# Kernel optimization log

Measured on AMD Instinct MI355X. Metric: run time of the kernel, lower is better.

## Reference

```python
import jax, jax.numpy as jnp
import numpy as np

B, L, H2 = 8, 512, 512  # batch, seq len (shared by a/b/c), 2*hidden


def setup_inputs() -> dict:
    key = jax.random.key(0)
    ka, kb, kc, kw1, kw2, kw3 = jax.random.split(key, 6)
    enc_a = jax.random.normal(ka, (B, L, H2), dtype=jnp.float32)
    enc_b = jax.random.normal(kb, (B, L, H2), dtype=jnp.float32)
    enc_c = jax.random.normal(kc, (B, L, H2), dtype=jnp.float32)
    # nn.Linear(6h, 1, bias=False) weight vectors; scaled so softmax isn't saturated
    w_ab = jax.random.normal(kw1, (3 * H2,), dtype=jnp.float32) * 0.02
    w_ac = jax.random.normal(kw2, (3 * H2,), dtype=jnp.float32) * 0.02
    w_bc = jax.random.normal(kw3, (3 * H2,), dtype=jnp.float32) * 0.02
    return {"encoded_a": enc_a, "encoded_b": enc_b, "encoded_c": enc_c,
            "w_ab": w_ab, "w_ac": w_ac, "w_bc": w_bc}


def _pair_att(A, Bx, w):
    """BiDAF-style pair attention.
    Original: S[b,i,j] = w . cat(A_i, B_j, A_i*B_j); here decomposed as
    S = A@w1 + B@w2 + A diag(w3) B^T  (identical math, no (B,La,Lb,6h) tensor).
    Returns a2b (B,La,2h) and b2a (B,2h) [pre-repeat].
    """
    h2 = A.shape[-1]
    wA, wB, wM = w[:h2], w[h2:2 * h2], w[2 * h2:]
    S = (A @ wA)[:, :, None] + (Bx @ wB)[:, None, :] \
        + jnp.einsum('bik,bjk->bij', A * wM, Bx)          # (B, La, Lb)
    a2b = jnp.einsum('bij,bjd->bid', jax.nn.softmax(S, axis=-1), Bx)  # (B, La, 2h)
    beta = jax.nn.softmax(jnp.max(S, axis=2), axis=-1)                # (B, La)
    b2a = jnp.einsum('bi,bid->bd', beta, A)                           # (B, 2h)
    return a2b, b2a


def reference(encoded_a, encoded_b, encoded_c, w_ab, w_ac, w_bc):
    b, len_b = encoded_b.shape[0], encoded_b.shape[1]
    len_c = encoded_c.shape[1]
    a2b, b2a = _pair_att(encoded_a, encoded_b, w_ab)
    a2c, c2a = _pair_att(encoded_a, encoded_c, w_ac)
    b2c, c2b = _pair_att(encoded_b, encoded_c, w_bc)
    # repeat the pooled vectors along the target sequence dim (as in torch .repeat)
    b2a = jnp.broadcast_to(b2a[:, None, :], (b, len_b, b2a.shape[-1]))
    c2a = jnp.broadcast_to(c2a[:, None, :], (b, len_c, c2a.shape[-1]))
    c2b = jnp.broadcast_to(c2b[:, None, :], (b, len_c, c2b.shape[-1]))
    att_a = jnp.concatenate((encoded_a, a2b, a2c, encoded_a * a2b, encoded_a * a2c), axis=2)
    att_b = jnp.concatenate((encoded_b, b2a, b2c, encoded_b * b2a, encoded_b * b2c), axis=2)
    att_c = jnp.concatenate((encoded_c, c2a, c2b, encoded_c * c2a, encoded_c * c2b), axis=2)
    return jnp.concatenate((att_a, att_b, att_c), axis=1)  # (B, La+Lb+Lc, 10h)
```

## Files before the change

kernel.cpp:

```cpp
#include <hip/hip_runtime.h>
#include <cmath>

#define BB 8
#define LL 512
#define HH 512

typedef __attribute__((ext_vector_type(8))) short short8;
typedef __attribute__((ext_vector_type(4))) float floatx4;

#define MM __builtin_amdgcn_mfma_f32_16x16x32_bf16
#define SB() __builtin_amdgcn_sched_barrier(0)

__device__ __forceinline__ unsigned short f2bf(float x) {
  unsigned int u = __float_as_uint(x);
  unsigned int r = (u + 0x7fffu + ((u >> 16) & 1u)) >> 16;
  return (unsigned short)r;
}

__global__ __launch_bounds__(256) void k0_conv(
    const float* __restrict__ Bm, const float* __restrict__ C,
    unsigned short* __restrict__ Bn, unsigned short* __restrict__ Cn,
    unsigned short* __restrict__ Bt, unsigned short* __restrict__ Ct) {
  __shared__ unsigned short tile[64][68];
  int bid = blockIdx.x;
  int s = bid >> 9;
  int rem = bid & 511;
  int b = rem >> 6, tr = (rem >> 3) & 7, tc = rem & 7;
  const float* src = s ? C : Bm;
  unsigned short* dn = s ? Cn : Bn;
  unsigned short* dt = s ? Ct : Bt;
  int t = threadIdx.x;
  int r0 = t >> 4, c0 = (t & 15) * 4;
#pragma unroll
  for (int rr = 0; rr < 4; ++rr) {
    int r = rr * 16 + r0;
    const float* sp = src + ((size_t)(b * 512 + tr * 64 + r)) * 512 + tc * 64 + c0;
    float4 v = *(const float4*)sp;
    unsigned short h0 = f2bf(v.x), h1 = f2bf(v.y), h2 = f2bf(v.z), h3 = f2bf(v.w);
    unsigned short* np = dn + ((size_t)(b * 512 + tr * 64 + r)) * 512 + tc * 64 + c0;
    np[0] = h0; np[1] = h1; np[2] = h2; np[3] = h3;
    tile[r][c0] = h0; tile[r][c0 + 1] = h1; tile[r][c0 + 2] = h2; tile[r][c0 + 3] = h3;
  }
  __syncthreads();
  int d = t & 63, j0 = (t >> 6) * 16;
  short8 v0, v1;
#pragma unroll
  for (int e = 0; e < 8; ++e) v0[e] = (short)tile[j0 + e][d];
#pragma unroll
  for (int e = 0; e < 8; ++e) v1[e] = (short)tile[j0 + 8 + e][d];
  unsigned short* tp = dt + ((size_t)(b * 512 + tc * 64 + d)) * 512 + tr * 64 + j0;
  *(short8*)tp = v0;
  *(short8*)(tp + 8) = v1;
}

__global__ __launch_bounds__(256) void k0_xm(
    const float* __restrict__ A, const float* __restrict__ Bm,
    const float* __restrict__ w0, const float* __restrict__ w1, const float* __restrict__ w2,
    unsigned short* __restrict__ Xm0, unsigned short* __restrict__ Xm1,
    unsigned short* __restrict__ Xm2) {
  unsigned int idx = blockIdx.x * 256 + threadIdx.x;
  size_t e0 = (size_t)idx * 8;
  int k0 = (int)(e0 & 511);
  unsigned int ri = (unsigned int)(e0 >> 9);
  int p = ri >> 12;
  unsigned int rowi = ri & 4095;
  const float* X = (p == 2) ? Bm : A;
  const float* wm = ((p == 0) ? w0 : (p == 1) ? w1 : w2) + 2 * HH;
  const float* xp = X + (size_t)rowi * 512 + k0;
  float4 a = *(const float4*)xp, b4 = *(const float4*)(xp + 4);
  float4 wa = *(const float4*)(wm + k0), wb = *(const float4*)(wm + k0 + 4);
  short8 o;
  o[0] = (short)f2bf(a.x * wa.x); o[1] = (short)f2bf(a.y * wa.y);
  o[2] = (short)f2bf(a.z * wa.z); o[3] = (short)f2bf(a.w * wa.w);
  o[4] = (short)f2bf(b4.x * wb.x); o[5] = (short)f2bf(b4.y * wb.y);
  o[6] = (short)f2bf(b4.z * wb.z); o[7] = (short)f2bf(b4.w * wb.w);
  unsigned short* op = ((p == 0) ? Xm0 : (p == 1) ? Xm1 : Xm2) + (size_t)rowi * 512 + k0;
  *(short8*)op = o;
}

__global__ __launch_bounds__(256) void k1_terms(
    const float* __restrict__ A, const float* __restrict__ Bm, const float* __restrict__ C,
    const float* __restrict__ w0, const float* __restrict__ w1, const float* __restrict__ w2,
    float* __restrict__ rowterm, float* __restrict__ colterm) {
  int tid = threadIdx.x;
  int wave = blockIdx.x * 4 + (tid >> 6);
  int lane = tid & 63;
  int m = wave >> 12;
  int rem = wave & 4095;
  int b = rem >> 9, i = rem & 511;
  const float* src = (m == 0) ? A : (m == 1 ? Bm : C);
  const float *wva, *wvb;
  float *da, *db;
  if (m == 0) {
    wva = w0;      wvb = w1;
    da = rowterm + (0 * BB + b) * LL + i;  db = rowterm + (1 * BB + b) * LL + i;
  } else if (m == 1) {
    wva = w0 + HH; wvb = w2;
    da = colterm + (0 * BB + b) * LL + i;  db = rowterm + (2 * BB + b) * LL + i;
  } else {
    wva = w1 + HH; wvb = w2 + HH;
    da = colterm + (1 * BB + b) * LL + i;  db = colterm + (2 * BB + b) * LL + i;
  }
  const float* row = src + ((size_t)b * LL + i) * HH;
  float a1 = 0.f, a2 = 0.f;
#pragma unroll
  for (int t = 0; t < 8; ++t) {
    float x = row[t * 64 + lane];
    a1 += x * wva[t * 64 + lane];
    a2 += x * wvb[t * 64 + lane];
  }
#pragma unroll
  for (int off = 32; off; off >>= 1) {
    a1 += __shfl_xor(a1, off, 64);
    a2 += __shfl_xor(a2, off, 64);
  }
  if (lane == 0) { *da = a1; *db = a2; }
}

__global__ __launch_bounds__(512, 2) void k2_mfma(
    const unsigned short* __restrict__ Xm0, const unsigned short* __restrict__ Xm1,
    const unsigned short* __restrict__ Xm2,
    const unsigned short* __restrict__ Bn, const unsigned short* __restrict__ Cn,
    const unsigned short* __restrict__ Bt, const unsigned short* __restrict__ Ct,
    const float* __restrict__ A, const float* __restrict__ Bm,
    const float* __restrict__ rowterm, const float* __restrict__ colterm,
    float* __restrict__ mrow, float* __restrict__ out) {
  __shared__ __align__(16) unsigned char smem[65536];
  unsigned short* A_lds = (unsigned short*)smem;
  unsigned short* P_lds = (unsigned short*)smem;
  float* sm_m = (float*)smem;
  float* sm_l = (float*)(smem + 2048);

  int tid = threadIdx.x;
  int bid0 = blockIdx.x;
  int bid = (bid0 & 7) * 24 + (bid0 >> 3);
  int p = bid >> 6;
  int b = (bid >> 3) & 7;
  int rb = bid & 7;
  int i0 = rb * 64;

  const unsigned short* Xmp = (p == 0) ? Xm0 : ((p == 1) ? Xm1 : Xm2);
  const unsigned short* Yn  = (p == 0) ? Bn : Cn;
  const unsigned short* Yt  = (p == 0) ? Bt : Ct;
  const float* X = (p == 2) ? Bm : A;

  int wc = tid >> 6;
  int lane = tid & 63;
  int n16 = lane & 15, q = lane >> 4;
  int e8 = n16 & 7;

#pragma unroll
  for (int j = 0; j < 8; ++j) {
    int idx = j * 512 + tid;
    int row = idx >> 6;
    int cc = idx & 63;
    short8 v = *(const short8*)(Xmp + ((size_t)(b * LL + i0 + row)) * HH + cc * 8);
    *(short8*)&A_lds[row * 512 + (cc ^ (row & 7)) * 8] = v;
  }
  __syncthreads();

  const unsigned short* br0 = Yn + ((size_t)(b * LL + wc * 64 + n16)) * HH + q * 8;
  const unsigned short* br1 = br0 + 16 * HH;
  const unsigned short* br2 = br0 + 32 * HH;
  const unsigned short* br3 = br0 + 48 * HH;

  floatx4 acc[4][4] = {};
  short8 Ax0[4], Ax1[4], Bx0[4], Bx1[4], Bx2[4];

#define LA(AF, kk) do { int ch_ = (((kk) * 4 + q) ^ e8) * 8; \
    AF[0] = *(const short8*)&A_lds[(n16)      * 512 + ch_]; \
    AF[1] = *(const short8*)&A_lds[(16 + n16) * 512 + ch_]; \
    AF[2] = *(const short8*)&A_lds[(32 + n16) * 512 + ch_]; \
    AF[3] = *(const short8*)&A_lds[(48 + n16) * 512 + ch_]; } while (0)
#define LB1(BF, kk) do { const int k0_ = (kk) * 32; \
    BF[0] = *(const short8*)(br0 + k0_); \
    BF[1] = *(const short8*)(br1 + k0_); \
    BF[2] = *(const short8*)(br2 + k0_); \
    BF[3] = *(const short8*)(br3 + k0_); } while (0)
#define MF1(AF, BF) do { \
    acc[0][0]=MM(AF[0],BF[0],acc[0][0],0,0,0); acc[0][1]=MM(AF[0],BF[1],acc[0][1],0,0,0); \
    acc[0][2]=MM(AF[0],BF[2],acc[0][2],0,0,0); acc[0][3]=MM(AF[0],BF[3],acc[0][3],0,0,0); \
    acc[1][0]=MM(AF[1],BF[0],acc[1][0],0,0,0); acc[1][1]=MM(AF[1],BF[1],acc[1][1],0,0,0); \
    acc[1][2]=MM(AF[1],BF[2],acc[1][2],0,0,0); acc[1][3]=MM(AF[1],BF[3],acc[1][3],0,0,0); \
    acc[2][0]=MM(AF[2],BF[0],acc[2][0],0,0,0); acc[2][1]=MM(AF[2],BF[1],acc[2][1],0,0,0); \
    acc[2][2]=MM(AF[2],BF[2],acc[2][2],0,0,0); acc[2][3]=MM(AF[2],BF[3],acc[2][3],0,0,0); \
    acc[3][0]=MM(AF[3],BF[0],acc[3][0],0,0,0); acc[3][1]=MM(AF[3],BF[1],acc[3][1],0,0,0); \
    acc[3][2]=MM(AF[3],BF[2],acc[3][2],0,0,0); acc[3][3]=MM(AF[3],BF[3],acc[3][3],0,0,0); } while (0)

  LB1(Bx0, 0); LB1(Bx1, 1); LB1(Bx2, 2); LA(Ax0, 0); LA(Ax1, 1); SB();
  MF1(Ax0, Bx0); LA(Ax0, 2);  LB1(Bx0, 3);  SB();
  MF1(Ax1, Bx1); LA(Ax1, 3);  LB1(Bx1, 4);  SB();
  MF1(Ax0, Bx2); LA(Ax0, 4);  LB1(Bx2, 5);  SB();
  MF1(Ax1, Bx0); LA(Ax1, 5);  LB1(Bx0, 6);  SB();
  MF1(Ax0, Bx1); LA(Ax0, 6);  LB1(Bx1, 7);  SB();
  MF1(Ax1, Bx2); LA(Ax1, 7);  LB1(Bx2, 8);  SB();
  MF1(Ax0, Bx0); LA(Ax0, 8);  LB1(Bx0, 9);  SB();
  MF1(Ax1, Bx1); LA(Ax1, 9);  LB1(Bx1, 10); SB();
  MF1(Ax0, Bx2); LA(Ax0, 10); LB1(Bx2, 11); SB();
  MF1(Ax1, Bx0); LA(Ax1, 11); LB1(Bx0, 12); SB();
  MF1(Ax0, Bx1); LA(Ax0, 12); LB1(Bx1, 13); SB();
  MF1(Ax1, Bx2); LA(Ax1, 13); LB1(Bx2, 14); SB();
  MF1(Ax0, Bx0); LA(Ax0, 14); LB1(Bx0, 15); SB();
  MF1(Ax1, Bx1); LA(Ax1, 15); SB();
  MF1(Ax0, Bx2); SB();
  MF1(Ax1, Bx0);
#undef LA
#undef LB1
#undef MF1

  __syncthreads();

  float rtv[4][4], ctv[4], mh[4][4], ml[4][4], rinv[4][4];
  {
    const float* rtp = rowterm + (p * BB + b) * LL + i0 + q * 4;
#pragma unroll
    for (int rt = 0; rt < 4; ++rt)
#pragma unroll
      for (int r = 0; r < 4; ++r) rtv[rt][r] = rtp[rt * 16 + r];
    const float* ctp = colterm + (p * BB + b) * LL + wc * 64 + n16;
#pragma unroll
    for (int f = 0; f < 4; ++f) ctv[f] = ctp[f * 16];
  }
#pragma unroll
  for (int rt = 0; rt < 4; ++rt)
#pragma unroll
    for (int r = 0; r < 4; ++r) {
      float m = -1e30f;
#pragma unroll
      for (int f = 0; f < 4; ++f) {
        float v = acc[rt][f][r] + rtv[rt][r] + ctv[f];
        acc[rt][f][r] = v;
        m = fmaxf(m, v);
      }
      m = fmaxf(m, __shfl_xor(m, 1, 64));
      m = fmaxf(m, __shfl_xor(m, 2, 64));
      m = fmaxf(m, __shfl_xor(m, 4, 64));
      m = fmaxf(m, __shfl_xor(m, 8, 64));
      mh[rt][r] = m;
    }
  if (n16 == 0) {
#pragma unroll
    for (int rt = 0; rt < 4; ++rt)
#pragma unroll
      for (int r = 0; r < 4; ++r) sm_m[wc * 64 + rt * 16 + q * 4 + r] = mh[rt][r];
  }
  __syncthreads();
#pragma unroll
  for (int rt = 0; rt < 4; ++rt)
#pragma unroll
    for (int r = 0; r < 4; ++r) {
      float m = mh[rt][r];
#pragma unroll
      for (int k = 0; k < 8; ++k) m = fmaxf(m, sm_m[k * 64 + rt * 16 + q * 4 + r]);
      mh[rt][r] = m;
      float l = 0.f;
#pragma unroll
      for (int f = 0; f < 4; ++f) {
        float pv = __expf(acc[rt][f][r] - m);
        acc[rt][f][r] = pv;
        l += pv;
      }
      l += __shfl_xor(l, 1, 64);
      l += __shfl_xor(l, 2, 64);
      l += __shfl_xor(l, 4, 64);
      l += __shfl_xor(l, 8, 64);
      ml[rt][r] = l;
    }
  if (n16 == 0) {
#pragma unroll
    for (int rt = 0; rt < 4; ++rt)
#pragma unroll
      for (int r = 0; r < 4; ++r) sm_l[wc * 64 + rt * 16 + q * 4 + r] = ml[rt][r];
    if (wc == 0) {
#pragma unroll
      for (int rt = 0; rt < 4; ++rt)
#pragma unroll
        for (int r = 0; r < 4; ++r)
          mrow[(p * BB + b) * LL + i0 + rt * 16 + q * 4 + r] = mh[rt][r];
    }
  }
  __syncthreads();
#pragma unroll
  for (int rt = 0; rt < 4; ++rt)
#pragma unroll
    for (int r = 0; r < 4; ++r) {
      float lf = 0.f;
#pragma unroll
      for (int k = 0; k < 8; ++k) lf += sm_l[k * 64 + rt * 16 + q * 4 + r];
      rinv[rt][r] = 1.f / lf;
    }
  __syncthreads();

#pragma unroll
  for (int f = 0; f < 4; ++f) {
    int c = wc * 8 + f * 2 + (n16 >> 3);
#pragma unroll
    for (int rt = 0; rt < 4; ++rt)
#pragma unroll
      for (int r = 0; r < 4; ++r) {
        int row = rt * 16 + q * 4 + r;
        int pc = c ^ (row & 7);
        P_lds[row * 512 + pc * 8 + e8] = f2bf(acc[rt][f][r]);
      }
  }
  __syncthreads();

  const unsigned short* tr0 = Yt + ((size_t)(b * LL + wc * 64 + n16)) * HH + q * 8;
  const unsigned short* tr1 = tr0 + 16 * HH;
  const unsigned short* tr2 = tr0 + 32 * HH;
  const unsigned short* tr3 = tr0 + 48 * HH;

  floatx4 oacc[4][4] = {};
  short8 Px0[4], Px1[4], By0[4], By1[4], By2[4];

#define LP(PF, kj) do { int ch_ = (((kj) * 4 + q) ^ e8) * 8; \
    PF[0] = *(const short8*)&P_lds[(n16)      * 512 + ch_]; \
    PF[1] = *(const short8*)&P_lds[(16 + n16) * 512 + ch_]; \
    PF[2] = *(const short8*)&P_lds[(32 + n16) * 512 + ch_]; \
    PF[3] = *(const short8*)&P_lds[(48 + n16) * 512 + ch_]; } while (0)
#define LB2(BF, kj) do { const int j0_ = (kj) * 32; \
    BF[0] = *(const short8*)(tr0 + j0_); \
    BF[1] = *(const short8*)(tr1 + j0_); \
    BF[2] = *(const short8*)(tr2 + j0_); \
    BF[3] = *(const short8*)(tr3 + j0_); } while (0)
#define MF2(PF, BF) do { \
    oacc[0][0]=MM(PF[0],BF[0],oacc[0][0],0,0,0); oacc[0][1]=MM(PF[0],BF[1],oacc[0][1],0,0,0); \
    oacc[0][2]=MM(PF[0],BF[2],oacc[0][2],0,0,0); oacc[0][3]=MM(PF[0],BF[3],oacc[0][3],0,0,0); \
    oacc[1][0]=MM(PF[1],BF[0],oacc[1][0],0,0,0); oacc[1][1]=MM(PF[1],BF[1],oacc[1][1],0,0,0); \
    oacc[1][2]=MM(PF[1],BF[2],oacc[1][2],0,0,0); oacc[1][3]=MM(PF[1],BF[3],oacc[1][3],0,0,0); \
    oacc[2][0]=MM(PF[2],BF[0],oacc[2][0],0,0,0); oacc[2][1]=MM(PF[2],BF[1],oacc[2][1],0,0,0); \
    oacc[2][2]=MM(PF[2],BF[2],oacc[2][2],0,0,0); oacc[2][3]=MM(PF[2],BF[3],oacc[2][3],0,0,0); \
    oacc[3][0]=MM(PF[3],BF[0],oacc[3][0],0,0,0); oacc[3][1]=MM(PF[3],BF[1],oacc[3][1],0,0,0); \
    oacc[3][2]=MM(PF[3],BF[2],oacc[3][2],0,0,0); oacc[3][3]=MM(PF[3],BF[3],oacc[3][3],0,0,0); } while (0)

  LB2(By0, 0); LB2(By1, 1); LB2(By2, 2); LP(Px0, 0); LP(Px1, 1); SB();
  MF2(Px0, By0); LP(Px0, 2);  LB2(By0, 3);  SB();
  MF2(Px1, By1); LP(Px1, 3);  LB2(By1, 4);  SB();
  MF2(Px0, By2); LP(Px0, 4);  LB2(By2, 5);  SB();
  MF2(Px1, By0); LP(Px1, 5);  LB2(By0, 6);  SB();
  MF2(Px0, By1); LP(Px0, 6);  LB2(By1, 7);  SB();
  MF2(Px1, By2); LP(Px1, 7);  LB2(By2, 8);  SB();
  MF2(Px0, By0); LP(Px0, 8);  LB2(By0, 9);  SB();
  MF2(Px1, By1); LP(Px1, 9);  LB2(By1, 10); SB();
  MF2(Px0, By2); LP(Px0, 10); LB2(By2, 11); SB();
  MF2(Px1, By0); LP(Px1, 11); LB2(By0, 12); SB();
  MF2(Px0, By1); LP(Px0, 12); LB2(By1, 13); SB();
  MF2(Px1, By2); LP(Px1, 13); LB2(By2, 14); SB();
  MF2(Px0, By0); LP(Px0, 14); LB2(By0, 15); SB();
  MF2(Px1, By1); LP(Px1, 15); SB();
  MF2(Px0, By2); SB();
  MF2(Px1, By0);
#undef LP
#undef LB2
#undef MF2

  int secoff, colbase;
  if      (p == 0) { secoff = 0;   colbase = 512;  }
  else if (p == 1) { secoff = 0;   colbase = 1024; }
  else             { secoff = 512; colbase = 1024; }

#pragma unroll
  for (int f = 0; f < 4; ++f) {
    int d = wc * 64 + f * 16 + n16;
#pragma unroll
    for (int rt = 0; rt < 4; ++rt)
#pragma unroll
      for (int r = 0; r < 4; ++r) {
        int ig = i0 + rt * 16 + q * 4 + r;
        float val = oacc[rt][f][r] * rinv[rt][r];
        size_t ob = ((size_t)b * 1536 + secoff + ig) * 2560;
        out[ob + colbase + d] = val;
        out[ob + colbase + 1024 + d] = X[((size_t)b * LL + ig) * HH + d] * val;
      }
  }
}

__global__ __launch_bounds__(256) void k3_beta(
    const float* __restrict__ A, const float* __restrict__ Bm,
    const float* __restrict__ mrow, float* __restrict__ vvec) {
  __shared__ float red[256];
  __shared__ float beta[LL];
  __shared__ float s_inv;
  int blk = blockIdx.x;
  int p = blk >> 6;
  int rem2 = blk & 63;
  int b = rem2 >> 3;
  int dch = rem2 & 7;
  int tid = threadIdx.x;
  const float* m = mrow + (p * BB + b) * LL;
  red[tid] = fmaxf(m[tid], m[tid + 256]);
  __syncthreads();
  for (int off = 128; off; off >>= 1) {
    if (tid < off) red[tid] = fmaxf(red[tid], red[tid + off]);
    __syncthreads();
  }
  float mx = red[0];
  __syncthreads();
  float e0 = __expf(m[tid] - mx), e1 = __expf(m[tid + 256] - mx);
  beta[tid] = e0; beta[tid + 256] = e1;
  red[tid] = e0 + e1;
  __syncthreads();
  for (int off = 128; off; off >>= 1) {
    if (tid < off) red[tid] += red[tid + off];
    __syncthreads();
  }
  if (tid == 0) s_inv = 1.f / red[0];
  __syncthreads();
  const float* Xb = ((p == 2) ? Bm : A) + (size_t)b * LL * HH;
  int d = dch * 64 + (tid & 63);
  int ig = tid >> 6;
  float acc = 0.f;
#pragma unroll 8
  for (int i = ig * 128; i < ig * 128 + 128; ++i)
    acc += beta[i] * Xb[(size_t)i * HH + d];
  red[tid] = acc;
  __syncthreads();
  if (tid < 64) {
    float s = red[tid] + red[tid + 64] + red[tid + 128] + red[tid + 192];
    vvec[(p * BB + b) * HH + dch * 64 + tid] = s * s_inv;
  }
}

__global__ __launch_bounds__(256) void k4_finalize(
    const float* __restrict__ A, const float* __restrict__ Bm, const float* __restrict__ C,
    const float* __restrict__ vvec, float* __restrict__ out) {
  unsigned int idx = blockIdx.x * 256 + threadIdx.x;
  int f4 = idx & 127;
  int i  = (idx >> 7) & 511;
  unsigned int ub = idx >> 16;
  unsigned int u = ub % 9;
  unsigned int b = ub / 9;
  int sec, slice;
  if (u == 0)      { sec = 0; slice = 0; }
  else if (u <= 3) { sec = 1; slice = (u == 1) ? 0 : (u == 2 ? 1 : 3); }
  else             { sec = 2; slice = (int)u - 4; }
  int cc = f4 * 4;
  const float* enc = sec == 0 ? A : (sec == 1 ? Bm : C);
  float4 val;
  if (slice == 0) {
    val = *(const float4*)(enc + ((size_t)b * LL + i) * HH + cc);
  } else {
    int vp = (sec == 1) ? 0 : ((slice == 1 || slice == 3) ? 1 : 2);
    float4 v = *(const float4*)(vvec + (vp * BB + b) * HH + cc);
    if (slice <= 2) {
      val = v;
    } else {
      float4 e = *(const float4*)(enc + ((size_t)b * LL + i) * HH + cc);
      val.x = e.x * v.x; val.y = e.y * v.y; val.z = e.z * v.z; val.w = e.w * v.w;
    }
  }
  *(float4*)(out + ((size_t)b * 1536 + sec * 512 + i) * 2560 + slice * 512 + cc) = val;
}

extern "C" void kernel_launch(void* const* d_in, const int* in_sizes, int n_in,
                              void* d_out, int out_size, void* d_ws, size_t ws_size,
                              hipStream_t stream) {
  const float* A  = (const float*)d_in[0];
  const float* Bm = (const float*)d_in[1];
  const float* C  = (const float*)d_in[2];
  const float* w0 = (const float*)d_in[3];
  const float* w1 = (const float*)d_in[4];
  const float* w2 = (const float*)d_in[5];
  float* out = (float*)d_out;

  float* wsf = (float*)d_ws;
  float* rowterm = wsf;
  float* colterm = wsf + 12288;
  float* mrow    = wsf + 24576;
  float* vvec    = wsf + 36864;
  unsigned short* wss = (unsigned short*)(wsf + 49152);
  const size_t MSZ = (size_t)BB * LL * HH;
  unsigned short* Bn  = wss;
  unsigned short* Cn  = wss + MSZ;
  unsigned short* Bt  = wss + 2 * MSZ;
  unsigned short* Ct  = wss + 3 * MSZ;
  unsigned short* Xm0 = wss + 4 * MSZ;
  unsigned short* Xm1 = wss + 5 * MSZ;
  unsigned short* Xm2 = wss + 6 * MSZ;

  k0_conv<<<1024, 256, 0, stream>>>(Bm, C, Bn, Cn, Bt, Ct);
  k0_xm<<<3072, 256, 0, stream>>>(A, Bm, w0, w1, w2, Xm0, Xm1, Xm2);
  k1_terms<<<3072, 256, 0, stream>>>(A, Bm, C, w0, w1, w2, rowterm, colterm);
  k2_mfma<<<192, 512, 0, stream>>>(Xm0, Xm1, Xm2, Bn, Cn, Bt, Ct, A, Bm,
                                   rowterm, colterm, mrow, out);
  k3_beta<<<192, 256, 0, stream>>>(A, Bm, mrow, vvec);
  k4_finalize<<<18432, 256, 0, stream>>>(A, Bm, C, vvec, out);
}
```

Measured before the change: 223.6 us.

## Fuse preprocessing passes and write encoder copies from the attention kernel

Merges the bf16 conversion, the Xm weight products and the row/column term dot products into a single pass that reads each fp32 row once with vectorized loads. The transpose kernel now reads bf16 instead of fp32. The attention kernel also writes the raw encoder slices for the a and b sections, which lets the finalize kernel drop two of its nine slice groups. k3_beta moves to 512 threads. The aim is to cut redundant fp32 reads of the inputs and extra output traffic, at the cost of more stores inside the MFMA kernel epilogue.

```diff
diff --git a/kernel.cpp b/kernel.cpp
--- a/kernel.cpp
+++ b/kernel.cpp
@@ -17,70 +17,12 @@
   return (unsigned short)r;
 }
 
-__global__ __launch_bounds__(256) void k0_conv(
-    const float* __restrict__ Bm, const float* __restrict__ C,
-    unsigned short* __restrict__ Bn, unsigned short* __restrict__ Cn,
-    unsigned short* __restrict__ Bt, unsigned short* __restrict__ Ct) {
-  __shared__ unsigned short tile[64][68];
-  int bid = blockIdx.x;
-  int s = bid >> 9;
-  int rem = bid & 511;
-  int b = rem >> 6, tr = (rem >> 3) & 7, tc = rem & 7;
-  const float* src = s ? C : Bm;
-  unsigned short* dn = s ? Cn : Bn;
-  unsigned short* dt = s ? Ct : Bt;
-  int t = threadIdx.x;
-  int r0 = t >> 4, c0 = (t & 15) * 4;
-#pragma unroll
-  for (int rr = 0; rr < 4; ++rr) {
-    int r = rr * 16 + r0;
-    const float* sp = src + ((size_t)(b * 512 + tr * 64 + r)) * 512 + tc * 64 + c0;
-    float4 v = *(const float4*)sp;
-    unsigned short h0 = f2bf(v.x), h1 = f2bf(v.y), h2 = f2bf(v.z), h3 = f2bf(v.w);
-    unsigned short* np = dn + ((size_t)(b * 512 + tr * 64 + r)) * 512 + tc * 64 + c0;
-    np[0] = h0; np[1] = h1; np[2] = h2; np[3] = h3;
-    tile[r][c0] = h0; tile[r][c0 + 1] = h1; tile[r][c0 + 2] = h2; tile[r][c0 + 3] = h3;
-  }
-  __syncthreads();
-  int d = t & 63, j0 = (t >> 6) * 16;
-  short8 v0, v1;
-#pragma unroll
-  for (int e = 0; e < 8; ++e) v0[e] = (short)tile[j0 + e][d];
-#pragma unroll
-  for (int e = 0; e < 8; ++e) v1[e] = (short)tile[j0 + 8 + e][d];
-  unsigned short* tp = dt + ((size_t)(b * 512 + tc * 64 + d)) * 512 + tr * 64 + j0;
-  *(short8*)tp = v0;
-  *(short8*)(tp + 8) = v1;
-}
-
-__global__ __launch_bounds__(256) void k0_xm(
-    const float* __restrict__ A, const float* __restrict__ Bm,
+__global__ __launch_bounds__(256) void kP1(
+    const float* __restrict__ A, const float* __restrict__ Bm, const float* __restrict__ C,
     const float* __restrict__ w0, const float* __restrict__ w1, const float* __restrict__ w2,
     unsigned short* __restrict__ Xm0, unsigned short* __restrict__ Xm1,
-    unsigned short* __restrict__ Xm2) {
-  unsigned int idx = blockIdx.x * 256 + threadIdx.x;
-  size_t e0 = (size_t)idx * 8;
-  int k0 = (int)(e0 & 511);
-  unsigned int ri = (unsigned int)(e0 >> 9);
-  int p = ri >> 12;
-  unsigned int rowi = ri & 4095;
-  const float* X = (p == 2) ? Bm : A;
-  const float* wm = ((p == 0) ? w0 : (p == 1) ? w1 : w2) + 2 * HH;
-  const float* xp = X + (size_t)rowi * 512 + k0;
-  float4 a = *(const float4*)xp, b4 = *(const float4*)(xp + 4);
-  float4 wa = *(const float4*)(wm + k0), wb = *(const float4*)(wm + k0 + 4);
-  short8 o;
-  o[0] = (short)f2bf(a.x * wa.x); o[1] = (short)f2bf(a.y * wa.y);
-  o[2] = (short)f2bf(a.z * wa.z); o[3] = (short)f2bf(a.w * wa.w);
-  o[4] = (short)f2bf(b4.x * wb.x); o[5] = (short)f2bf(b4.y * wb.y);
-  o[6] = (short)f2bf(b4.z * wb.z); o[7] = (short)f2bf(b4.w * wb.w);
-  unsigned short* op = ((p == 0) ? Xm0 : (p == 1) ? Xm1 : Xm2) + (size_t)rowi * 512 + k0;
-  *(short8*)op = o;
-}
-
-__global__ __launch_bounds__(256) void k1_terms(
-    const float* __restrict__ A, const float* __restrict__ Bm, const float* __restrict__ C,
-    const float* __restrict__ w0, const float* __restrict__ w1, const float* __restrict__ w2,
+    unsigned short* __restrict__ Xm2,
+    unsigned short* __restrict__ Bn, unsigned short* __restrict__ Cn,
     float* __restrict__ rowterm, float* __restrict__ colterm) {
   int tid = threadIdx.x;
   int wave = blockIdx.x * 4 + (tid >> 6);
@@ -89,6 +31,10 @@
   int rem = wave & 4095;
   int b = rem >> 9, i = rem & 511;
   const float* src = (m == 0) ? A : (m == 1 ? Bm : C);
+  const float* rp = src + (size_t)rem * HH + lane * 8;
+  float4 xa = *(const float4*)rp, xb = *(const float4*)(rp + 4);
+  float x[8] = {xa.x, xa.y, xa.z, xa.w, xb.x, xb.y, xb.z, xb.w};
+
   const float *wva, *wvb;
   float *da, *db;
   if (m == 0) {
@@ -101,20 +47,80 @@
     wva = w1 + HH; wvb = w2 + HH;
     da = colterm + (1 * BB + b) * LL + i;  db = colterm + (2 * BB + b) * LL + i;
   }
-  const float* row = src + ((size_t)b * LL + i) * HH;
+  const float* ap1 = wva + lane * 8;
+  const float* bp1 = wvb + lane * 8;
+  float4 wa1 = *(const float4*)ap1, wa2 = *(const float4*)(ap1 + 4);
+  float4 wb1 = *(const float4*)bp1, wb2 = *(const float4*)(bp1 + 4);
+  float wa[8] = {wa1.x, wa1.y, wa1.z, wa1.w, wa2.x, wa2.y, wa2.z, wa2.w};
+  float wb[8] = {wb1.x, wb1.y, wb1.z, wb1.w, wb2.x, wb2.y, wb2.z, wb2.w};
   float a1 = 0.f, a2 = 0.f;
 #pragma unroll
-  for (int t = 0; t < 8; ++t) {
-    float x = row[t * 64 + lane];
-    a1 += x * wva[t * 64 + lane];
-    a2 += x * wvb[t * 64 + lane];
-  }
+  for (int e = 0; e < 8; ++e) { a1 += x[e] * wa[e]; a2 += x[e] * wb[e]; }
 #pragma unroll
   for (int off = 32; off; off >>= 1) {
     a1 += __shfl_xor(a1, off, 64);
     a2 += __shfl_xor(a2, off, 64);
   }
   if (lane == 0) { *da = a1; *db = a2; }
+
+  size_t oo = (size_t)rem * HH + lane * 8;
+  if (m == 0) {
+    const float* m0 = w0 + 2 * HH + lane * 8;
+    const float* m1 = w1 + 2 * HH + lane * 8;
+    float4 ma1 = *(const float4*)m0, ma2 = *(const float4*)(m0 + 4);
+    float4 mb1 = *(const float4*)m1, mb2 = *(const float4*)(m1 + 4);
+    float wm0[8] = {ma1.x, ma1.y, ma1.z, ma1.w, ma2.x, ma2.y, ma2.z, ma2.w};
+    float wm1[8] = {mb1.x, mb1.y, mb1.z, mb1.w, mb2.x, mb2.y, mb2.z, mb2.w};
+    short8 o0, o1;
+#pragma unroll
+    for (int e = 0; e < 8; ++e) { o0[e] = (short)f2bf(x[e] * wm0[e]); o1[e] = (short)f2bf(x[e] * wm1[e]); }
+    *(short8*)(Xm0 + oo) = o0;
+    *(short8*)(Xm1 + oo) = o1;
+  } else if (m == 1) {
+    const float* m2 = w2 + 2 * HH + lane * 8;
+    float4 mc1 = *(const float4*)m2, mc2 = *(const float4*)(m2 + 4);
+    float wm2[8] = {mc1.x, mc1.y, mc1.z, mc1.w, mc2.x, mc2.y, mc2.z, mc2.w};
+    short8 on, o2;
+#pragma unroll
+    for (int e = 0; e < 8; ++e) { on[e] = (short)f2bf(x[e]); o2[e] = (short)f2bf(x[e] * wm2[e]); }
+    *(short8*)(Bn + oo) = on;
+    *(short8*)(Xm2 + oo) = o2;
+  } else {
+    short8 on;
+#pragma unroll
+    for (int e = 0; e < 8; ++e) on[e] = (short)f2bf(x[e]);
+    *(short8*)(Cn + oo) = on;
+  }
+}
+
+__global__ __launch_bounds__(256) void k0t(
+    const unsigned short* __restrict__ Bn, const unsigned short* __restrict__ Cn,
+    unsigned short* __restrict__ Bt, unsigned short* __restrict__ Ct) {
+  __shared__ unsigned short tile[64][68];
+  int bid = blockIdx.x;
+  int s = bid >> 9;
+  int rem = bid & 511;
+  int b = rem >> 6, tr = (rem >> 3) & 7, tc = rem & 7;
+  const unsigned short* src = s ? Cn : Bn;
+  unsigned short* dt = s ? Ct : Bt;
+  int t = threadIdx.x;
+#pragma unroll
+  for (int h = 0; h < 2; ++h) {
+    int id = h * 256 + t;
+    int row = id >> 3, c8 = id & 7;
+    short8 v = *(const short8*)(src + ((size_t)(b * 512 + tr * 64 + row)) * 512 + tc * 64 + c8 * 8);
+    *(short8*)&tile[row][c8 * 8] = v;
+  }
+  __syncthreads();
+  int d = t >> 2, jc = t & 3;
+  short8 v0, v1;
+#pragma unroll
+  for (int e = 0; e < 8; ++e) v0[e] = (short)tile[jc * 16 + e][d];
+#pragma unroll
+  for (int e = 0; e < 8; ++e) v1[e] = (short)tile[jc * 16 + 8 + e][d];
+  unsigned short* tp = dt + ((size_t)(b * 512 + tc * 64 + d)) * 512 + tr * 64 + jc * 16;
+  *(short8*)tp = v0;
+  *(short8*)(tp + 8) = v1;
 }
 
 __global__ __launch_bounds__(512, 2) void k2_mfma(
@@ -369,16 +375,19 @@
         int ig = i0 + rt * 16 + q * 4 + r;
         float val = oacc[rt][f][r] * rinv[rt][r];
         size_t ob = ((size_t)b * 1536 + secoff + ig) * 2560;
+        float xv = X[((size_t)b * LL + ig) * HH + d];
         out[ob + colbase + d] = val;
-        out[ob + colbase + 1024 + d] = X[((size_t)b * LL + ig) * HH + d] * val;
+        out[ob + colbase + 1024 + d] = xv * val;
+        if (p == 0) out[ob + d] = xv;
+        if (p == 2) out[ob + d] = xv;
       }
   }
 }
 
-__global__ __launch_bounds__(256) void k3_beta(
+__global__ __launch_bounds__(512) void k3_beta(
     const float* __restrict__ A, const float* __restrict__ Bm,
     const float* __restrict__ mrow, float* __restrict__ vvec) {
-  __shared__ float red[256];
+  __shared__ float red[512];
   __shared__ float beta[LL];
   __shared__ float s_inv;
   int blk = blockIdx.x;
@@ -388,19 +397,19 @@
   int dch = rem2 & 7;
   int tid = threadIdx.x;
   const float* m = mrow + (p * BB + b) * LL;
-  red[tid] = fmaxf(m[tid], m[tid + 256]);
-  __syncthreads();
-  for (int off = 128; off; off >>= 1) {
+  red[tid] = m[tid];
+  __syncthreads();
+  for (int off = 256; off; off >>= 1) {
     if (tid < off) red[tid] = fmaxf(red[tid], red[tid + off]);
     __syncthreads();
   }
   float mx = red[0];
   __syncthreads();
-  float e0 = __expf(m[tid] - mx), e1 = __expf(m[tid + 256] - mx);
-  beta[tid] = e0; beta[tid + 256] = e1;
-  red[tid] = e0 + e1;
-  __syncthreads();
-  for (int off = 128; off; off >>= 1) {
+  float e0 = __expf(m[tid] - mx);
+  beta[tid] = e0;
+  red[tid] = e0;
+  __syncthreads();
+  for (int off = 256; off; off >>= 1) {
     if (tid < off) red[tid] += red[tid + off];
     __syncthreads();
   }
@@ -410,13 +419,15 @@
   int d = dch * 64 + (tid & 63);
   int ig = tid >> 6;
   float acc = 0.f;
-#pragma unroll 8
-  for (int i = ig * 128; i < ig * 128 + 128; ++i)
-    acc += beta[i] * Xb[(size_t)i * HH + d];
+#pragma unroll 4
+  for (int i2 = ig * 64; i2 < ig * 64 + 64; ++i2)
+    acc += beta[i2] * Xb[(size_t)i2 * HH + d];
   red[tid] = acc;
   __syncthreads();
   if (tid < 64) {
-    float s = red[tid] + red[tid + 64] + red[tid + 128] + red[tid + 192];
+    float s = 0.f;
+#pragma unroll
+    for (int k = 0; k < 8; ++k) s += red[tid + k * 64];
     vvec[(p * BB + b) * HH + dch * 64 + tid] = s * s_inv;
   }
 }
@@ -428,26 +439,29 @@
   int f4 = idx & 127;
   int i  = (idx >> 7) & 511;
   unsigned int ub = idx >> 16;
-  unsigned int u = ub % 9;
-  unsigned int b = ub / 9;
-  int sec, slice;
-  if (u == 0)      { sec = 0; slice = 0; }
-  else if (u <= 3) { sec = 1; slice = (u == 1) ? 0 : (u == 2 ? 1 : 3); }
-  else             { sec = 2; slice = (int)u - 4; }
+  unsigned int u = ub % 7;
+  unsigned int b = ub / 7;
+  int sec, slice, mode = 0, vp = 0;
+  const float* enc = C;
+  switch (u) {
+    case 0: sec = 1; slice = 1; mode = 0; vp = 0; break;
+    case 1: sec = 1; slice = 3; mode = 1; vp = 0; enc = Bm; break;
+    case 2: sec = 2; slice = 0; mode = 2; break;
+    case 3: sec = 2; slice = 1; mode = 0; vp = 1; break;
+    case 4: sec = 2; slice = 2; mode = 0; vp = 2; break;
+    case 5: sec = 2; slice = 3; mode = 1; vp = 1; break;
+    default: sec = 2; slice = 4; mode = 1; vp = 2; break;
+  }
   int cc = f4 * 4;
-  const float* enc = sec == 0 ? A : (sec == 1 ? Bm : C);
   float4 val;
-  if (slice == 0) {
+  if (mode == 0) {
+    val = *(const float4*)(vvec + (vp * BB + b) * HH + cc);
+  } else if (mode == 2) {
     val = *(const float4*)(enc + ((size_t)b * LL + i) * HH + cc);
   } else {
-    int vp = (sec == 1) ? 0 : ((slice == 1 || slice == 3) ? 1 : 2);
     float4 v = *(const float4*)(vvec + (vp * BB + b) * HH + cc);
-    if (slice <= 2) {
-      val = v;
-    } else {
-      float4 e = *(const float4*)(enc + ((size_t)b * LL + i) * HH + cc);
-      val.x = e.x * v.x; val.y = e.y * v.y; val.z = e.z * v.z; val.w = e.w * v.w;
-    }
+    float4 e = *(const float4*)(enc + ((size_t)b * LL + i) * HH + cc);
+    val.x = e.x * v.x; val.y = e.y * v.y; val.z = e.z * v.z; val.w = e.w * v.w;
   }
   *(float4*)(out + ((size_t)b * 1536 + sec * 512 + i) * 2560 + slice * 512 + cc) = val;
 }
@@ -478,11 +492,11 @@
   unsigned short* Xm1 = wss + 5 * MSZ;
   unsigned short* Xm2 = wss + 6 * MSZ;
 
-  k0_conv<<<1024, 256, 0, stream>>>(Bm, C, Bn, Cn, Bt, Ct);
-  k0_xm<<<3072, 256, 0, stream>>>(A, Bm, w0, w1, w2, Xm0, Xm1, Xm2);
-  k1_terms<<<3072, 256, 0, stream>>>(A, Bm, C, w0, w1, w2, rowterm, colterm);
+  kP1<<<3072, 256, 0, stream>>>(A, Bm, C, w0, w1, w2, Xm0, Xm1, Xm2, Bn, Cn,
+                                rowterm, colterm);
+  k0t<<<1024, 256, 0, stream>>>(Bn, Cn, Bt, Ct);
   k2_mfma<<<192, 512, 0, stream>>>(Xm0, Xm1, Xm2, Bn, Cn, Bt, Ct, A, Bm,
                                    rowterm, colterm, mrow, out);
-  k3_beta<<<192, 256, 0, stream>>>(A, Bm, mrow, vvec);
-  k4_finalize<<<18432, 256, 0, stream>>>(A, Bm, C, vvec, out);
-}
+  k3_beta<<<192, 512, 0, stream>>>(A, Bm, mrow, vvec);
+  k4_finalize<<<14336, 256, 0, stream>>>(A, Bm, C, vvec, out);
+}
```

After: 240.1 us. +7.4%, slower.
